# Performance work log

Hardware: AMD Instinct MI355X
Metric: run time of the kernel (lower is better)

## Reference

```python
import jax, jax.numpy as jnp
import numpy as np

LATENT = 1024
TEXT = 768
HEADS = 16
HEAD_DIM = LATENT // HEADS
SCALE = HEAD_DIM ** -0.5
LN_EPS = 1e-5


def setup_inputs() -> dict:
    key = jax.random.key(0)
    ks = jax.random.split(key, 16)
    B, Tx, Txf = 4, 4096, 256
    def lin(k, fan_in, fan_out):
        bound = 1.0 / np.sqrt(fan_in)
        kw, kb = jax.random.split(k)
        W = jax.random.uniform(kw, (fan_in, fan_out), jnp.float32, -bound, bound)
        b = jax.random.uniform(kb, (fan_out,), jnp.float32, -bound, bound)
        return W, b
    Wq, bq = lin(ks[0], LATENT, LATENT)
    Wk, bk = lin(ks[1], TEXT, LATENT)
    Wv, bv = lin(ks[2], TEXT, LATENT)
    Wo, bo = lin(ks[3], LATENT, LATENT)
    W1, b1 = lin(ks[4], LATENT, 4 * LATENT)
    W2, b2 = lin(ks[5], 4 * LATENT, LATENT)
    return {
        "x": jax.random.normal(ks[6], (B, Tx, LATENT), jnp.float32),
        "xf": jax.random.normal(ks[7], (B, Txf, TEXT), jnp.float32),
        "Wq": Wq, "bq": bq, "Wk": Wk, "bk": bk, "Wv": Wv, "bv": bv,
        "Wo": Wo, "bo": bo,
        "ln_g": jnp.ones((LATENT,), jnp.float32),
        "ln_b": jnp.zeros((LATENT,), jnp.float32),
        "W1": W1, "b1": b1, "W2": W2, "b2": b2,
    }


def reference(x, xf, Wq, bq, Wk, bk, Wv, bv, Wo, bo, ln_g, ln_b, W1, b1, W2, b2):
    B, Tx, D = x.shape
    Txf = xf.shape[1]
    # projections -> [B, H, T, Dh]
    q = (x @ Wq + bq).reshape(B, Tx, HEADS, HEAD_DIM).transpose(0, 2, 1, 3)
    k = (xf @ Wk + bk).reshape(B, Txf, HEADS, HEAD_DIM).transpose(0, 2, 1, 3)
    v = (xf @ Wv + bv).reshape(B, Txf, HEADS, HEAD_DIM).transpose(0, 2, 1, 3)
    # chunked loop in original == full softmax over keys (dropout=0 at eval)
    scores = jnp.einsum('bhqd,bhkd->bhqk', q * SCALE, k)
    probs = jax.nn.softmax(scores, axis=-1)
    attn = jnp.einsum('bhqk,bhkd->bhqd', probs, v)
    out = attn.transpose(0, 2, 1, 3).reshape(B, Tx, D)
    out = out @ Wo + bo
    # FFN: LayerNorm -> Linear -> GELU(exact) -> Linear
    mu = jnp.mean(out, axis=-1, keepdims=True)
    var = jnp.var(out, axis=-1, keepdims=True)
    h = (out - mu) * jax.lax.rsqrt(var + LN_EPS) * ln_g + ln_b
    h = jax.nn.gelu(h @ W1 + b1, approximate=False)
    ffn = h @ W2 + b2
    out = out + ffn
    return x + out
```

## Files before the change

kernel.cpp:

```cpp
#include <hip/hip_runtime.h>
#include <hip/hip_bf16.h>
#include <cmath>

typedef __bf16 bf16_t;
typedef __bf16 bf16x8 __attribute__((ext_vector_type(8)));
typedef __bf16 bf16x4 __attribute__((ext_vector_type(4)));
typedef float f32x4 __attribute__((ext_vector_type(4)));

#define LATENT 1024
#define HEADS 16
#define HD 64
#define TX 4096
#define TXF 256
#define SCALE_ATTN 0.125f

static __device__ __forceinline__ float b2f(bf16_t b) { return (float)b; }
static __device__ __forceinline__ bf16_t f2b(float f) { return (bf16_t)f; }

static __device__ __forceinline__ void glds16(const bf16_t* g, bf16_t* l) {
    __builtin_amdgcn_global_load_lds(
        (const __attribute__((address_space(1))) void*)g,
        (__attribute__((address_space(3))) void*)l, 16, 0, 0);
}

__global__ __launch_bounds__(256) void cvt_k(const float* __restrict__ in,
                                             bf16_t* __restrict__ out, long n4) {
    long i = (long)blockIdx.x * 256 + threadIdx.x;
    long stride = (long)gridDim.x * 256;
    for (; i < n4; i += stride) {
        float4 v = ((const float4*)in)[i];
        bf16x4 o;
        o[0] = f2b(v.x); o[1] = f2b(v.y); o[2] = f2b(v.z); o[3] = f2b(v.w);
        *(bf16x4*)&out[i * 4] = o;
    }
}

__global__ __launch_bounds__(256) void tr_k(const float* __restrict__ in,
                                            bf16_t* __restrict__ out,
                                            int R, int C) {
    __shared__ float t[32][33];
    int bx = blockIdx.x, by = blockIdx.y;
    int x = threadIdx.x & 31, y0 = threadIdx.x >> 5;
    for (int i = 0; i < 32; i += 8)
        t[y0 + i][x] = in[(long)(by * 32 + y0 + i) * C + bx * 32 + x];
    __syncthreads();
    for (int i = 0; i < 32; i += 8)
        out[(long)(bx * 32 + y0 + i) * R + by * 32 + x] = f2b(t[x][y0 + i]);
}

template <int EPI>
__global__ __launch_bounds__(256, 2) void gemm_k(
    const bf16_t* __restrict__ A, const bf16_t* __restrict__ Bt,
    const float* __restrict__ bias, void* __restrict__ C,
    const bf16_t* __restrict__ resb16, const float* __restrict__ resf32,
    int M, int N, int K) {
    __shared__ __align__(16) bf16_t As[128 * 64];
    __shared__ __align__(16) bf16_t Bs[128 * 64];
    int tid = threadIdx.x;
    int lane = tid & 63, wid = tid >> 6;
    int quad = lane >> 4, l16 = lane & 15;
    int wm = wid >> 1, wn = wid & 1;
    int srow0 = wid * 8 + (lane >> 3);
    int schunk = (lane & 7) ^ (lane >> 3);

    f32x4 acc[4][4] = {};
    long bm = blockIdx.x, bn = blockIdx.y;
    const bf16_t* Ab = A + (bm * 128 + srow0) * (long)K + schunk * 8;
    const bf16_t* Bb = Bt + (bn * 128 + srow0) * (long)K + schunk * 8;
    bf16_t* AsD = As + wid * 512;
    bf16_t* BsD = Bs + wid * 512;

    for (int k0 = 0; k0 < K; k0 += 64) {
        __syncthreads();
#pragma unroll
        for (int t = 0; t < 4; t++) {
            glds16(Ab + k0 + (long)t * 32 * K, AsD + t * 2048);
            glds16(Bb + k0 + (long)t * 32 * K, BsD + t * 2048);
        }
        __syncthreads();
#pragma unroll
        for (int s = 0; s < 2; s++) {
            bf16x8 af[4], bfr[4];
#pragma unroll
            for (int mi = 0; mi < 4; mi++) {
                int r = wm * 64 + mi * 16 + l16;
                af[mi] = *(const bf16x8*)&As[r * 64 + (((s * 4 + quad) ^ (r & 7)) * 8)];
            }
#pragma unroll
            for (int ni = 0; ni < 4; ni++) {
                int r = wn * 64 + ni * 16 + l16;
                bfr[ni] = *(const bf16x8*)&Bs[r * 64 + (((s * 4 + quad) ^ (r & 7)) * 8)];
            }
#pragma unroll
            for (int mi = 0; mi < 4; mi++)
#pragma unroll
                for (int ni = 0; ni < 4; ni++)
                    acc[mi][ni] = __builtin_amdgcn_mfma_f32_16x16x32_bf16(
                        af[mi], bfr[ni], acc[mi][ni], 0, 0, 0);
        }
    }

    int colb = (int)bn * 128 + wn * 64;
    float bvv[4];
#pragma unroll
    for (int ni = 0; ni < 4; ni++) bvv[ni] = bias[colb + ni * 16 + l16];
#pragma unroll
    for (int mi = 0; mi < 4; mi++) {
        long grow = bm * 128 + wm * 64 + mi * 16 + quad * 4;
#pragma unroll
        for (int r = 0; r < 4; r++) {
            long ro = (grow + r) * (long)N;
#pragma unroll
            for (int ni = 0; ni < 4; ni++) {
                long idx = ro + colb + ni * 16 + l16;
                float v = acc[mi][ni][r] + bvv[ni];
                if (EPI == 0) {
                    ((bf16_t*)C)[idx] = f2b(v);
                } else if (EPI == 2) {
                    ((bf16_t*)C)[idx] =
                        f2b(0.5f * v * (1.0f + erff(v * 0.70710678118f)));
                } else {
                    ((float*)C)[idx] = v + b2f(resb16[idx]) + resf32[idx];
                }
            }
        }
    }
}

__global__ __launch_bounds__(256, 2) void attn_k(const bf16_t* __restrict__ Q,
                                                 const bf16_t* __restrict__ Kb,
                                                 const bf16_t* __restrict__ Vb,
                                                 bf16_t* __restrict__ Ob) {
    __shared__ __align__(16) bf16_t SM[32768];
    bf16_t* Ks = SM;
    bf16_t* Vt = SM + 16384;
    int tid = threadIdx.x;
    int lane = tid & 63, w = tid >> 6;
    int quad = lane >> 4, l16 = lane & 15;
    int qt = blockIdx.x & 63;
    int bh = blockIdx.x >> 6;
    int b = bh >> 4, h = bh & 15;

    {
        const uint4* ks = (const uint4*)(Kb + ((long)(b * TXF + tid) * LATENT + h * HD));
#pragma unroll
        for (int cc = 0; cc < 8; cc++)
            *(uint4*)&Ks[tid * 64 + ((cc ^ (tid & 7)) * 8)] = ks[cc];
        const uint4* vs = (const uint4*)(Vb + ((long)(b * TXF + tid) * LATENT + h * HD));
#pragma unroll
        for (int cc = 0; cc < 8; cc++) {
            uint4 v = vs[cc];
            const bf16_t* e = (const bf16_t*)&v;
#pragma unroll
            for (int j = 0; j < 8; j++) {
                int d = cc * 8 + j;
                Vt[d * 256 + (((tid >> 3) ^ (d & 7)) * 8) + (tid & 7)] = e[j];
            }
        }
    }
    long qrow = (long)(b * TX + qt * 64 + w * 16 + l16) * LATENT + h * HD;
    bf16x8 aq0 = *(const bf16x8*)(Q + qrow + quad * 8);
    bf16x8 aq1 = *(const bf16x8*)(Q + qrow + 32 + quad * 8);
    __syncthreads();

    f32x4 sacc[16] = {};
#pragma unroll
    for (int ni = 0; ni < 16; ni++) {
        int kr = ni * 16 + l16;
        bf16x8 b0 = *(const bf16x8*)&Ks[kr * 64 + ((quad ^ (kr & 7)) * 8)];
        bf16x8 b1 = *(const bf16x8*)&Ks[kr * 64 + (((4 + quad) ^ (kr & 7)) * 8)];
        sacc[ni] = __builtin_amdgcn_mfma_f32_16x16x32_bf16(aq0, b0, sacc[ni], 0, 0, 0);
        sacc[ni] = __builtin_amdgcn_mfma_f32_16x16x32_bf16(aq1, b1, sacc[ni], 0, 0, 0);
    }
#pragma unroll
    for (int r = 0; r < 4; r++) {
        float m = -3e38f;
#pragma unroll
        for (int ni = 0; ni < 16; ni++) m = fmaxf(m, sacc[ni][r]);
#pragma unroll
        for (int off = 1; off < 16; off <<= 1) m = fmaxf(m, __shfl_xor(m, off, 64));
        float s = 0.f;
#pragma unroll
        for (int ni = 0; ni < 16; ni++) {
            float p = __expf((sacc[ni][r] - m) * SCALE_ATTN);
            sacc[ni][r] = p;
            s += p;
        }
#pragma unroll
        for (int off = 1; off < 16; off <<= 1) s += __shfl_xor(s, off, 64);
        float inv = 1.0f / s;
#pragma unroll
        for (int ni = 0; ni < 16; ni++) sacc[ni][r] *= inv;
    }
    __syncthreads();

    bf16_t* Ps = SM;
#pragma unroll
    for (int r = 0; r < 4; r++) {
        int row = w * 16 + quad * 4 + r;
#pragma unroll
        for (int ni = 0; ni < 16; ni++) {
            int col = ni * 16 + l16;
            Ps[row * 256 + (((col >> 3) ^ (row & 7)) * 8) + (col & 7)] =
                f2b(sacc[ni][r]);
        }
    }
    __syncthreads();

    f32x4 oacc[4] = {};
#pragma unroll
    for (int s = 0; s < 8; s++) {
        int prow = w * 16 + l16;
        bf16x8 ap = *(const bf16x8*)&Ps[prow * 256 + (((s * 4 + quad) ^ (prow & 7)) * 8)];
#pragma unroll
        for (int ni = 0; ni < 4; ni++) {
            int vr = ni * 16 + l16;
            bf16x8 bv = *(const bf16x8*)&Vt[vr * 256 + (((s * 4 + quad) ^ (vr & 7)) * 8)];
            oacc[ni] = __builtin_amdgcn_mfma_f32_16x16x32_bf16(ap, bv, oacc[ni], 0, 0, 0);
        }
    }
#pragma unroll
    for (int r = 0; r < 4; r++) {
        long orow = (long)(b * TX + qt * 64 + w * 16 + quad * 4 + r) * LATENT + h * HD;
#pragma unroll
        for (int ni = 0; ni < 4; ni++)
            Ob[orow + ni * 16 + l16] = f2b(oacc[ni][r]);
    }
}

__global__ __launch_bounds__(256) void ln_k(const bf16_t* __restrict__ O,
                                            const float* __restrict__ g,
                                            const float* __restrict__ bb,
                                            bf16_t* __restrict__ H) {
    long row = blockIdx.x;
    int c = threadIdx.x * 4;
    bf16x4 v = *(const bf16x4*)(O + row * LATENT + c);
    float vv[4] = {b2f(v[0]), b2f(v[1]), b2f(v[2]), b2f(v[3])};
    float s = vv[0] + vv[1] + vv[2] + vv[3];
    float s2 = vv[0] * vv[0] + vv[1] * vv[1] + vv[2] * vv[2] + vv[3] * vv[3];
#pragma unroll
    for (int off = 1; off < 64; off <<= 1) {
        s += __shfl_xor(s, off, 64);
        s2 += __shfl_xor(s2, off, 64);
    }
    __shared__ float red[8];
    int lane = threadIdx.x & 63, w = threadIdx.x >> 6;
    if (lane == 0) { red[w] = s; red[w + 4] = s2; }
    __syncthreads();
    s = red[0] + red[1] + red[2] + red[3];
    s2 = red[4] + red[5] + red[6] + red[7];
    float mu = s * (1.0f / 1024.0f);
    float var = s2 * (1.0f / 1024.0f) - mu * mu;
    float rstd = rsqrtf(var + 1e-5f);
    bf16_t* out = H + row * LATENT + c;
#pragma unroll
    for (int j = 0; j < 4; j++)
        out[j] = f2b((vv[j] - mu) * rstd * g[c + j] + bb[c + j]);
}

extern "C" void kernel_launch(void* const* d_in, const int* in_sizes, int n_in,
                              void* d_out, int out_size, void* d_ws,
                              size_t ws_size, hipStream_t stream) {
    const float* x = (const float*)d_in[0];
    const float* xf = (const float*)d_in[1];
    const float* Wq = (const float*)d_in[2];
    const float* bq = (const float*)d_in[3];
    const float* Wk = (const float*)d_in[4];
    const float* bk = (const float*)d_in[5];
    const float* Wv = (const float*)d_in[6];
    const float* bv = (const float*)d_in[7];
    const float* Wo = (const float*)d_in[8];
    const float* bo = (const float*)d_in[9];
    const float* lng = (const float*)d_in[10];
    const float* lnb = (const float*)d_in[11];
    const float* W1 = (const float*)d_in[12];
    const float* b1 = (const float*)d_in[13];
    const float* W2 = (const float*)d_in[14];
    const float* b2 = (const float*)d_in[15];

    char* ws = (char*)d_ws;
    size_t off = 0;
    auto alloc = [&](size_t bytes) {
        void* p = ws + off;
        off += (bytes + 255) & ~(size_t)255;
        return p;
    };
    bf16_t* WqT = (bf16_t*)alloc((size_t)1024 * 1024 * 2);
    bf16_t* WkT = (bf16_t*)alloc((size_t)1024 * 768 * 2);
    bf16_t* WvT = (bf16_t*)alloc((size_t)1024 * 768 * 2);
    bf16_t* WoT = (bf16_t*)alloc((size_t)1024 * 1024 * 2);
    bf16_t* W1T = (bf16_t*)alloc((size_t)4096 * 1024 * 2);
    bf16_t* W2T = (bf16_t*)alloc((size_t)1024 * 4096 * 2);
    bf16_t* Obuf = (bf16_t*)alloc((size_t)16384 * 1024 * 2);
    bf16_t* Hbuf = (bf16_t*)alloc((size_t)16384 * 1024 * 2);
    size_t transient0 = off;
    bf16_t* xc = (bf16_t*)alloc((size_t)16384 * 1024 * 2);
    bf16_t* xfc = (bf16_t*)alloc((size_t)1024 * 768 * 2);
    bf16_t* Qbuf = (bf16_t*)alloc((size_t)16384 * 1024 * 2);
    bf16_t* Kbuf = (bf16_t*)alloc((size_t)1024 * 1024 * 2);
    bf16_t* Vbuf = (bf16_t*)alloc((size_t)1024 * 1024 * 2);
    bf16_t* Abuf = (bf16_t*)alloc((size_t)16384 * 1024 * 2);
    bf16_t* H1 = (bf16_t*)(ws + transient0);

    dim3 blk(256);
    cvt_k<<<dim3(4096), blk, 0, stream>>>(x, xc, (long)16384 * 1024 / 4);
    cvt_k<<<dim3(768), blk, 0, stream>>>(xf, xfc, (long)1024 * 768 / 4);
    tr_k<<<dim3(32, 32), blk, 0, stream>>>(Wq, WqT, 1024, 1024);
    tr_k<<<dim3(32, 24), blk, 0, stream>>>(Wk, WkT, 768, 1024);
    tr_k<<<dim3(32, 24), blk, 0, stream>>>(Wv, WvT, 768, 1024);
    tr_k<<<dim3(32, 32), blk, 0, stream>>>(Wo, WoT, 1024, 1024);
    tr_k<<<dim3(128, 32), blk, 0, stream>>>(W1, W1T, 1024, 4096);
    tr_k<<<dim3(32, 128), blk, 0, stream>>>(W2, W2T, 4096, 1024);

    gemm_k<0><<<dim3(128, 8), blk, 0, stream>>>(xc, WqT, bq, Qbuf, nullptr, nullptr, 16384, 1024, 1024);
    gemm_k<0><<<dim3(8, 8), blk, 0, stream>>>(xfc, WkT, bk, Kbuf, nullptr, nullptr, 1024, 1024, 768);
    gemm_k<0><<<dim3(8, 8), blk, 0, stream>>>(xfc, WvT, bv, Vbuf, nullptr, nullptr, 1024, 1024, 768);
    attn_k<<<dim3(4096), blk, 0, stream>>>(Qbuf, Kbuf, Vbuf, Abuf);
    gemm_k<0><<<dim3(128, 8), blk, 0, stream>>>(Abuf, WoT, bo, Obuf, nullptr, nullptr, 16384, 1024, 1024);
    ln_k<<<dim3(16384), blk, 0, stream>>>(Obuf, lng, lnb, Hbuf);
    gemm_k<2><<<dim3(128, 32), blk, 0, stream>>>(Hbuf, W1T, b1, H1, nullptr, nullptr, 16384, 4096, 1024);
    gemm_k<3><<<dim3(128, 8), blk, 0, stream>>>(H1, W2T, b2, d_out, Obuf, x, 16384, 1024, 4096);
}
```

Baseline: 652.7 us.

## Add 256x256-tile 8-wave GEMM with staged prefetch for large projections

Measured after the change: 679.8 us. 1.04x slower.

```diff
diff --git a/kernel.cpp b/kernel.cpp
--- a/kernel.cpp
+++ b/kernel.cpp
@@ -22,6 +22,8 @@
         (const __attribute__((address_space(1))) void*)g,
         (__attribute__((address_space(3))) void*)l, 16, 0, 0);
 }
+
+#define MFMA16(a, b, c) __builtin_amdgcn_mfma_f32_16x16x32_bf16(a, b, c, 0, 0, 0)
 
 __global__ __launch_bounds__(256) void cvt_k(const float* __restrict__ in,
                                              bf16_t* __restrict__ out, long n4) {
@@ -95,8 +97,7 @@
             for (int mi = 0; mi < 4; mi++)
 #pragma unroll
                 for (int ni = 0; ni < 4; ni++)
-                    acc[mi][ni] = __builtin_amdgcn_mfma_f32_16x16x32_bf16(
-                        af[mi], bfr[ni], acc[mi][ni], 0, 0, 0);
+                    acc[mi][ni] = MFMA16(af[mi], bfr[ni], acc[mi][ni]);
         }
     }
 
@@ -112,6 +113,153 @@
             long ro = (grow + r) * (long)N;
 #pragma unroll
             for (int ni = 0; ni < 4; ni++) {
+                long idx = ro + colb + ni * 16 + l16;
+                float v = acc[mi][ni][r] + bvv[ni];
+                if (EPI == 0) {
+                    ((bf16_t*)C)[idx] = f2b(v);
+                } else if (EPI == 2) {
+                    ((bf16_t*)C)[idx] =
+                        f2b(0.5f * v * (1.0f + erff(v * 0.70710678118f)));
+                } else {
+                    ((float*)C)[idx] = v + b2f(resb16[idx]) + resf32[idx];
+                }
+            }
+        }
+    }
+}
+
+template <int EPI>
+__global__ __launch_bounds__(512, 2) void gemm256_k(
+    const bf16_t* __restrict__ A, const bf16_t* __restrict__ Bt,
+    const float* __restrict__ bias, void* __restrict__ C,
+    const bf16_t* __restrict__ resb16, const float* __restrict__ resf32,
+    int M, int N, int K) {
+    __shared__ __align__(16) bf16_t As[2 * 16384];
+    __shared__ __align__(16) bf16_t Bs[2 * 16384];
+    int tid = threadIdx.x;
+    int lane = tid & 63, wid = tid >> 6;
+    int quad = lane >> 4, l16 = lane & 15;
+    int wm = wid >> 2, wn = wid & 3;
+    long bm = blockIdx.x, bn = blockIdx.y;
+    int NT = K >> 6;
+
+    int srow = wid * 8 + (lane >> 3);
+    int schunk = ((lane & 7) ^ (lane >> 3)) * 8;
+    const bf16_t* Asrc = A + (bm * 256 + srow) * (long)K + schunk;
+    const bf16_t* Bsrc = Bt + (bn * 256 + srow) * (long)K + schunk;
+
+    auto stageA = [&](int t, int r) {
+        glds16(Asrc + ((long)t * 64 + (long)r * 64 * K),
+               As + ((t & 1) * 16384 + r * 4096 + wid * 512));
+    };
+    auto stageB = [&](int t, int r) {
+        glds16(Bsrc + ((long)t * 64 + (long)r * 64 * K),
+               Bs + ((t & 1) * 16384 + r * 4096 + wid * 512));
+    };
+
+    stageA(0, 0); stageA(0, 1); stageA(0, 2); stageA(0, 3);
+    stageB(0, 0); stageB(0, 1); stageB(0, 2); stageB(0, 3);
+    stageA(1, 0); stageA(1, 1); stageA(1, 2); stageA(1, 3);
+    f32x4 acc[8][4] = {};
+    bf16x8 af[4][2], bq0[2][2], bq1[2][2];
+    asm volatile("s_waitcnt vmcnt(4)" ::: "memory");
+    __builtin_amdgcn_s_barrier();
+
+    for (int t = 0; t < NT; ++t) {
+        int cur = t & 1;
+        const bf16_t* AL = As + cur * 16384;
+        const bf16_t* BL = Bs + cur * 16384;
+#pragma unroll
+        for (int mi = 0; mi < 4; ++mi) {
+            int r = wm * 128 + mi * 16 + l16;
+            af[mi][0] = *(const bf16x8*)&AL[r * 64 + ((quad ^ (r & 7)) * 8)];
+            af[mi][1] = *(const bf16x8*)&AL[r * 64 + (((4 + quad) ^ (r & 7)) * 8)];
+        }
+#pragma unroll
+        for (int ni = 0; ni < 2; ++ni) {
+            int r = wn * 64 + ni * 16 + l16;
+            bq0[ni][0] = *(const bf16x8*)&BL[r * 64 + ((quad ^ (r & 7)) * 8)];
+            bq0[ni][1] = *(const bf16x8*)&BL[r * 64 + (((4 + quad) ^ (r & 7)) * 8)];
+        }
+        if (t + 1 < NT) { stageB(t + 1, 0); stageB(t + 1, 1); }
+        __builtin_amdgcn_s_barrier();
+        __builtin_amdgcn_s_setprio(1);
+#pragma unroll
+        for (int mi = 0; mi < 4; ++mi)
+#pragma unroll
+            for (int ni = 0; ni < 2; ++ni) {
+                acc[mi][ni] = MFMA16(af[mi][0], bq0[ni][0], acc[mi][ni]);
+                acc[mi][ni] = MFMA16(af[mi][1], bq0[ni][1], acc[mi][ni]);
+            }
+        __builtin_amdgcn_s_setprio(0);
+        __builtin_amdgcn_s_barrier();
+#pragma unroll
+        for (int ni = 0; ni < 2; ++ni) {
+            int r = wn * 64 + 32 + ni * 16 + l16;
+            bq1[ni][0] = *(const bf16x8*)&BL[r * 64 + ((quad ^ (r & 7)) * 8)];
+            bq1[ni][1] = *(const bf16x8*)&BL[r * 64 + (((4 + quad) ^ (r & 7)) * 8)];
+        }
+        if (t + 2 < NT) { stageA(t + 2, 0); stageA(t + 2, 2); }
+        __builtin_amdgcn_s_barrier();
+        __builtin_amdgcn_s_setprio(1);
+#pragma unroll
+        for (int mi = 0; mi < 4; ++mi)
+#pragma unroll
+            for (int ni = 0; ni < 2; ++ni) {
+                acc[mi][2 + ni] = MFMA16(af[mi][0], bq1[ni][0], acc[mi][2 + ni]);
+                acc[mi][2 + ni] = MFMA16(af[mi][1], bq1[ni][1], acc[mi][2 + ni]);
+            }
+        __builtin_amdgcn_s_setprio(0);
+        __builtin_amdgcn_s_barrier();
+#pragma unroll
+        for (int mi = 0; mi < 4; ++mi) {
+            int r = wm * 128 + 64 + mi * 16 + l16;
+            af[mi][0] = *(const bf16x8*)&AL[r * 64 + ((quad ^ (r & 7)) * 8)];
+            af[mi][1] = *(const bf16x8*)&AL[r * 64 + (((4 + quad) ^ (r & 7)) * 8)];
+        }
+        if (t + 1 < NT) { stageB(t + 1, 2); stageB(t + 1, 3); }
+        __builtin_amdgcn_s_barrier();
+        __builtin_amdgcn_s_setprio(1);
+#pragma unroll
+        for (int mi = 0; mi < 4; ++mi)
+#pragma unroll
+            for (int ni = 0; ni < 2; ++ni) {
+                acc[4 + mi][ni] = MFMA16(af[mi][0], bq0[ni][0], acc[4 + mi][ni]);
+                acc[4 + mi][ni] = MFMA16(af[mi][1], bq0[ni][1], acc[4 + mi][ni]);
+            }
+        __builtin_amdgcn_s_setprio(0);
+        __builtin_amdgcn_s_barrier();
+        if (t + 2 < NT) { stageA(t + 2, 1); stageA(t + 2, 3); }
+        __builtin_amdgcn_s_barrier();
+        __builtin_amdgcn_s_setprio(1);
+#pragma unroll
+        for (int mi = 0; mi < 4; ++mi)
+#pragma unroll
+            for (int ni = 0; ni < 2; ++ni) {
+                acc[4 + mi][2 + ni] = MFMA16(af[mi][0], bq1[ni][0], acc[4 + mi][2 + ni]);
+                acc[4 + mi][2 + ni] = MFMA16(af[mi][1], bq1[ni][1], acc[4 + mi][2 + ni]);
+            }
+        __builtin_amdgcn_s_setprio(0);
+        if (t + 2 < NT) {
+            asm volatile("s_waitcnt vmcnt(2)" ::: "memory");
+        } else if (t + 1 < NT) {
+            asm volatile("s_waitcnt vmcnt(0)" ::: "memory");
+        }
+        __builtin_amdgcn_s_barrier();
+    }
+
+    int colb = (int)bn * 256 + wn * 64;
+    float bvv[4];
+#pragma unroll
+    for (int ni = 0; ni < 4; ++ni) bvv[ni] = bias[colb + ni * 16 + l16];
+#pragma unroll
+    for (int mi = 0; mi < 8; ++mi) {
+        long grow = bm * 256 + wm * 128 + mi * 16 + quad * 4;
+#pragma unroll
+        for (int r = 0; r < 4; ++r) {
+            long ro = (grow + r) * (long)N;
+#pragma unroll
+            for (int ni = 0; ni < 4; ++ni) {
                 long idx = ro + colb + ni * 16 + l16;
                 float v = acc[mi][ni][r] + bvv[ni];
                 if (EPI == 0) {
@@ -169,8 +317,8 @@
         int kr = ni * 16 + l16;
         bf16x8 b0 = *(const bf16x8*)&Ks[kr * 64 + ((quad ^ (kr & 7)) * 8)];
         bf16x8 b1 = *(const bf16x8*)&Ks[kr * 64 + (((4 + quad) ^ (kr & 7)) * 8)];
-        sacc[ni] = __builtin_amdgcn_mfma_f32_16x16x32_bf16(aq0, b0, sacc[ni], 0, 0, 0);
-        sacc[ni] = __builtin_amdgcn_mfma_f32_16x16x32_bf16(aq1, b1, sacc[ni], 0, 0, 0);
+        sacc[ni] = MFMA16(aq0, b0, sacc[ni]);
+        sacc[ni] = MFMA16(aq1, b1, sacc[ni]);
     }
 #pragma unroll
     for (int r = 0; r < 4; r++) {
@@ -216,7 +364,7 @@
         for (int ni = 0; ni < 4; ni++) {
             int vr = ni * 16 + l16;
             bf16x8 bv = *(const bf16x8*)&Vt[vr * 256 + (((s * 4 + quad) ^ (vr & 7)) * 8)];
-            oacc[ni] = __builtin_amdgcn_mfma_f32_16x16x32_bf16(ap, bv, oacc[ni], 0, 0, 0);
+            oacc[ni] = MFMA16(ap, bv, oacc[ni]);
         }
     }
 #pragma unroll
@@ -302,7 +450,7 @@
     bf16_t* Abuf = (bf16_t*)alloc((size_t)16384 * 1024 * 2);
     bf16_t* H1 = (bf16_t*)(ws + transient0);
 
-    dim3 blk(256);
+    dim3 blk(256), blk5(512);
     cvt_k<<<dim3(4096), blk, 0, stream>>>(x, xc, (long)16384 * 1024 / 4);
     cvt_k<<<dim3(768), blk, 0, stream>>>(xf, xfc, (long)1024 * 768 / 4);
     tr_k<<<dim3(32, 32), blk, 0, stream>>>(Wq, WqT, 1024, 1024);
@@ -312,12 +460,12 @@
     tr_k<<<dim3(128, 32), blk, 0, stream>>>(W1, W1T, 1024, 4096);
     tr_k<<<dim3(32, 128), blk, 0, stream>>>(W2, W2T, 4096, 1024);
 
-    gemm_k<0><<<dim3(128, 8), blk, 0, stream>>>(xc, WqT, bq, Qbuf, nullptr, nullptr, 16384, 1024, 1024);
+    gemm256_k<0><<<dim3(64, 4), blk5, 0, stream>>>(xc, WqT, bq, Qbuf, nullptr, nullptr, 16384, 1024, 1024);
     gemm_k<0><<<dim3(8, 8), blk, 0, stream>>>(xfc, WkT, bk, Kbuf, nullptr, nullptr, 1024, 1024, 768);
     gemm_k<0><<<dim3(8, 8), blk, 0, stream>>>(xfc, WvT, bv, Vbuf, nullptr, nullptr, 1024, 1024, 768);
     attn_k<<<dim3(4096), blk, 0, stream>>>(Qbuf, Kbuf, Vbuf, Abuf);
-    gemm_k<0><<<dim3(128, 8), blk, 0, stream>>>(Abuf, WoT, bo, Obuf, nullptr, nullptr, 16384, 1024, 1024);
+    gemm256_k<0><<<dim3(64, 4), blk5, 0, stream>>>(Abuf, WoT, bo, Obuf, nullptr, nullptr, 16384, 1024, 1024);
     ln_k<<<dim3(16384), blk, 0, stream>>>(Obuf, lng, lnb, Hbuf);
-    gemm_k<2><<<dim3(128, 32), blk, 0, stream>>>(Hbuf, W1T, b1, H1, nullptr, nullptr, 16384, 4096, 1024);
-    gemm_k<3><<<dim3(128, 8), blk, 0, stream>>>(H1, W2T, b2, d_out, Obuf, x, 16384, 1024, 4096);
-}
+    gemm256_k<2><<<dim3(64, 16), blk5, 0, stream>>>(Hbuf, W1T, b1, H1, nullptr, nullptr, 16384, 4096, 1024);
+    gemm256_k<3><<<dim3(64, 4), blk5, 0, stream>>>(H1, W2T, b2, d_out, Obuf, x, 16384, 1024, 4096);
+}
```

## Swizzle GEMM workgroups across XCDs and merge weight transposes into one launch

Applied to the files above, without the earlier changes.

Result: slower. 732.8 us (+12.3%).

```diff
diff --git a/kernel.cpp b/kernel.cpp
--- a/kernel.cpp
+++ b/kernel.cpp
@@ -22,6 +22,8 @@
         (const __attribute__((address_space(1))) void*)g,
         (__attribute__((address_space(3))) void*)l, 16, 0, 0);
 }
+
+#define MFMA16(a, b, c) __builtin_amdgcn_mfma_f32_16x16x32_bf16(a, b, c, 0, 0, 0)
 
 __global__ __launch_bounds__(256) void cvt_k(const float* __restrict__ in,
                                              bf16_t* __restrict__ out, long n4) {
@@ -35,17 +37,28 @@
     }
 }
 
-__global__ __launch_bounds__(256) void tr_k(const float* __restrict__ in,
-                                            bf16_t* __restrict__ out,
-                                            int R, int C) {
+__global__ __launch_bounds__(256) void tr6_k(
+    const float* __restrict__ s0, bf16_t* __restrict__ d0,
+    const float* __restrict__ s1, bf16_t* __restrict__ d1,
+    const float* __restrict__ s2, bf16_t* __restrict__ d2,
+    const float* __restrict__ s3, bf16_t* __restrict__ d3,
+    const float* __restrict__ s4, bf16_t* __restrict__ d4,
+    const float* __restrict__ s5, bf16_t* __restrict__ d5) {
+    int id = blockIdx.x;
+    const float* src; bf16_t* dst; int R, C, bx, by;
+    if (id < 1024)      { src = s0; dst = d0; R = 1024; C = 1024; bx = id & 31;  by = id >> 5; }
+    else if (id < 1792) { id -= 1024; src = s1; dst = d1; R = 768;  C = 1024; bx = id & 31;  by = id >> 5; }
+    else if (id < 2560) { id -= 1792; src = s2; dst = d2; R = 768;  C = 1024; bx = id & 31;  by = id >> 5; }
+    else if (id < 3584) { id -= 2560; src = s3; dst = d3; R = 1024; C = 1024; bx = id & 31;  by = id >> 5; }
+    else if (id < 7680) { id -= 3584; src = s4; dst = d4; R = 1024; C = 4096; bx = id & 127; by = id >> 7; }
+    else                { id -= 7680; src = s5; dst = d5; R = 4096; C = 1024; bx = id & 31;  by = id >> 5; }
     __shared__ float t[32][33];
-    int bx = blockIdx.x, by = blockIdx.y;
     int x = threadIdx.x & 31, y0 = threadIdx.x >> 5;
     for (int i = 0; i < 32; i += 8)
-        t[y0 + i][x] = in[(long)(by * 32 + y0 + i) * C + bx * 32 + x];
+        t[y0 + i][x] = src[(long)(by * 32 + y0 + i) * C + bx * 32 + x];
     __syncthreads();
     for (int i = 0; i < 32; i += 8)
-        out[(long)(bx * 32 + y0 + i) * R + by * 32 + x] = f2b(t[x][y0 + i]);
+        dst[(long)(bx * 32 + y0 + i) * R + by * 32 + x] = f2b(t[x][y0 + i]);
 }
 
 template <int EPI>
@@ -63,8 +76,14 @@
     int srow0 = wid * 8 + (lane >> 3);
     int schunk = (lane & 7) ^ (lane >> 3);
 
+    int nwg = gridDim.x * gridDim.y;
+    int wgid = blockIdx.y * gridDim.x + blockIdx.x;
+    int cpx = nwg >> 3;
+    int swz = (wgid & 7) * cpx + (wgid >> 3);
+    long bm = swz % gridDim.x;
+    long bn = swz / gridDim.x;
+
     f32x4 acc[4][4] = {};
-    long bm = blockIdx.x, bn = blockIdx.y;
     const bf16_t* Ab = A + (bm * 128 + srow0) * (long)K + schunk * 8;
     const bf16_t* Bb = Bt + (bn * 128 + srow0) * (long)K + schunk * 8;
     bf16_t* AsD = As + wid * 512;
@@ -95,8 +114,7 @@
             for (int mi = 0; mi < 4; mi++)
 #pragma unroll
                 for (int ni = 0; ni < 4; ni++)
-                    acc[mi][ni] = __builtin_amdgcn_mfma_f32_16x16x32_bf16(
-                        af[mi], bfr[ni], acc[mi][ni], 0, 0, 0);
+                    acc[mi][ni] = MFMA16(af[mi], bfr[ni], acc[mi][ni]);
         }
     }
 
@@ -169,8 +187,8 @@
         int kr = ni * 16 + l16;
         bf16x8 b0 = *(const bf16x8*)&Ks[kr * 64 + ((quad ^ (kr & 7)) * 8)];
         bf16x8 b1 = *(const bf16x8*)&Ks[kr * 64 + (((4 + quad) ^ (kr & 7)) * 8)];
-        sacc[ni] = __builtin_amdgcn_mfma_f32_16x16x32_bf16(aq0, b0, sacc[ni], 0, 0, 0);
-        sacc[ni] = __builtin_amdgcn_mfma_f32_16x16x32_bf16(aq1, b1, sacc[ni], 0, 0, 0);
+        sacc[ni] = MFMA16(aq0, b0, sacc[ni]);
+        sacc[ni] = MFMA16(aq1, b1, sacc[ni]);
     }
 #pragma unroll
     for (int r = 0; r < 4; r++) {
@@ -216,7 +234,7 @@
         for (int ni = 0; ni < 4; ni++) {
             int vr = ni * 16 + l16;
             bf16x8 bv = *(const bf16x8*)&Vt[vr * 256 + (((s * 4 + quad) ^ (vr & 7)) * 8)];
-            oacc[ni] = __builtin_amdgcn_mfma_f32_16x16x32_bf16(ap, bv, oacc[ni], 0, 0, 0);
+            oacc[ni] = MFMA16(ap, bv, oacc[ni]);
         }
     }
 #pragma unroll
@@ -305,12 +323,8 @@
     dim3 blk(256);
     cvt_k<<<dim3(4096), blk, 0, stream>>>(x, xc, (long)16384 * 1024 / 4);
     cvt_k<<<dim3(768), blk, 0, stream>>>(xf, xfc, (long)1024 * 768 / 4);
-    tr_k<<<dim3(32, 32), blk, 0, stream>>>(Wq, WqT, 1024, 1024);
-    tr_k<<<dim3(32, 24), blk, 0, stream>>>(Wk, WkT, 768, 1024);
-    tr_k<<<dim3(32, 24), blk, 0, stream>>>(Wv, WvT, 768, 1024);
-    tr_k<<<dim3(32, 32), blk, 0, stream>>>(Wo, WoT, 1024, 1024);
-    tr_k<<<dim3(128, 32), blk, 0, stream>>>(W1, W1T, 1024, 4096);
-    tr_k<<<dim3(32, 128), blk, 0, stream>>>(W2, W2T, 4096, 1024);
+    tr6_k<<<dim3(11776), blk, 0, stream>>>(Wq, WqT, Wk, WkT, Wv, WvT,
+                                           Wo, WoT, W1, W1T, W2, W2T);
 
     gemm_k<0><<<dim3(128, 8), blk, 0, stream>>>(xc, WqT, bq, Qbuf, nullptr, nullptr, 16384, 1024, 1024);
     gemm_k<0><<<dim3(8, 8), blk, 0, stream>>>(xfc, WkT, bk, Kbuf, nullptr, nullptr, 1024, 1024, 768);
```
